# Kernel tuning notes

Measured on AMD Instinct MI355X. Metric: run time of the kernel, lower is better.

## Reference

```python
import jax, jax.numpy as jnp
import numpy as np

B, C, ROWS, COLS = 16, 1, 128, 128
E, H, L, VOCAB = 64, 32, 3, 258


def setup_inputs() -> dict:
    key = jax.random.key(0)
    ks = jax.random.split(key, 18)
    s = 0.05
    d = {
        "x": jax.random.randint(ks[0], (B, C, ROWS, COLS), 0, VOCAB, dtype=jnp.int32),
        "embed_table": jax.random.normal(ks[1], (VOCAB, E), jnp.float32) * s,
    }
    in_sizes = [E + 1, H, H]
    k = 2
    for l in range(L):
        d[f"w_ih_l{l}"] = jax.random.normal(ks[k], (3 * H, in_sizes[l]), jnp.float32) * s; k += 1
        d[f"w_hh_l{l}"] = jax.random.normal(ks[k], (3 * H, H), jnp.float32) * s; k += 1
        d[f"b_ih_l{l}"] = jax.random.normal(ks[k], (3 * H,), jnp.float32) * s; k += 1
        d[f"b_hh_l{l}"] = jax.random.normal(ks[k], (3 * H,), jnp.float32) * s; k += 1
    d["w_h2e"] = jax.random.normal(ks[14], (E + 1, H), jnp.float32) * s
    d["b_h2e"] = jax.random.normal(ks[15], (E + 1,), jnp.float32) * s
    d["w_out"] = jax.random.normal(ks[16], (VOCAB, H), jnp.float32) * s
    d["b_out"] = jax.random.normal(ks[17], (VOCAB,), jnp.float32) * s
    return d


def _forward(x, embed_table, wih, whh, bih, bhh, w_h2e, b_h2e, w_out, b_out):
    b, c, rows, cols = x.shape
    T = cols * c  # GRU sequence length per row
    Hh = whh[0].shape[1]
    nL = len(wih)

    xf = x.reshape(b, rows, T)
    emb = embed_table[xf]  # [B, rows, T, E]
    # normalized row coordinate in [-1, 1), appended as extra feature
    row_pos = jnp.arange(rows, dtype=emb.dtype) / rows * 2.0 - 1.0
    row_feat = jnp.broadcast_to(row_pos[None, :, None, None], (b, rows, T, 1))
    xin = jnp.concatenate([emb, row_feat], axis=-1)  # [B, rows, T, E+1]

    def gru_step(h, x_t):
        # h: [L, B, H]; x_t: [B, E+1]. torch GRU gate order: r, z, n.
        inp = x_t
        hs = []
        for l in range(nL):
            gi = inp @ wih[l].T + bih[l]
            gh = h[l] @ whh[l].T + bhh[l]
            ir, iz, inn = jnp.split(gi, 3, axis=-1)
            hr, hz, hn = jnp.split(gh, 3, axis=-1)
            r = jax.nn.sigmoid(ir + hr)
            z = jax.nn.sigmoid(iz + hz)
            n = jnp.tanh(inn + r * hn)
            hl = (1.0 - z) * n + z * h[l]
            hs.append(hl)
            inp = hl
        return jnp.stack(hs), inp  # emit top-layer output

    def row_step(prev_out, x_row):
        # prev_out: [B, T, H] top-layer GRU output of previous row
        comb = x_row + prev_out @ w_h2e.T + b_h2e  # [B, T, E+1]
        h0 = jnp.zeros((nL, b, Hh), comb.dtype)  # fresh h0 per row, as in torch
        _, out = jax.lax.scan(gru_step, h0, jnp.swapaxes(comb, 0, 1))  # [T, B, H]
        out = jnp.swapaxes(out, 0, 1)  # [B, T, H]
        return out, out

    prev0 = jnp.zeros((b, T, Hh), xin.dtype)
    _, outs = jax.lax.scan(row_step, prev0, jnp.swapaxes(xin, 0, 1))  # [rows, B, T, H]
    outs = jnp.swapaxes(outs, 0, 1)  # [B, rows, T, H]
    pred = outs @ w_out.T + b_out  # [B, rows, T, 258]
    return pred.reshape(b, c, rows, cols, VOCAB)


def reference(x, embed_table, w_ih_l0, w_hh_l0, b_ih_l0, b_hh_l0,
              w_ih_l1, w_hh_l1, b_ih_l1, b_hh_l1,
              w_ih_l2, w_hh_l2, b_ih_l2, b_hh_l2,
              w_h2e, b_h2e, w_out, b_out):
    return _forward(x, embed_table,
                    (w_ih_l0, w_ih_l1, w_ih_l2),
                    (w_hh_l0, w_hh_l1, w_hh_l2),
                    (b_ih_l0, b_ih_l1, b_ih_l2),
                    (b_hh_l0, b_hh_l1, b_hh_l2),
                    w_h2e, b_h2e, w_out, b_out)
```

## Files before the change

### kernel.cpp

```cpp
#include <hip/hip_runtime.h>
#include <math.h>

#define BATCH 16
#define RWS   128
#define TT    128
#define HH    32
#define GG    96
#define RPB   8
#define NRG   (RWS/RPB)
#define WSTR  34
#define FSTR  16

#define H2_BYTES   (BATCH*RWS*TT*HH*4)
#define FLAG_OFF   H2_BYTES
#define FLAG_BYTES (NRG*BATCH*FSTR*4)
#define PTAB_OFF   (FLAG_OFF + FLAG_BYTES)
#define WF_OFF     (PTAB_OFF + 258*GG*4)

__device__ __forceinline__ float sigm(float x) { return 1.0f / (1.0f + __expf(-x)); }
__device__ __forceinline__ float tanhfast(float x) {
  x = fminf(fmaxf(x, -15.0f), 15.0f);
  float e = __expf(2.0f * x);
  return (e - 1.0f) / (e + 1.0f);
}

__device__ __forceinline__ float dot32(const float* __restrict__ w, const float* __restrict__ v) {
  float a0 = 0.f, a1 = 0.f;
#pragma unroll
  for (int k = 0; k < HH; k += 4) {
    float2 w0 = *(const float2*)(w + k);
    float2 w1 = *(const float2*)(w + k + 2);
    float2 v0 = *(const float2*)(v + k);
    float2 v1 = *(const float2*)(v + k + 2);
    a0 = fmaf(w0.x, v0.x, fmaf(w0.y, v0.y, a0));
    a1 = fmaf(w1.x, v1.x, fmaf(w1.y, v1.y, a1));
  }
  return a0 + a1;
}

__global__ __launch_bounds__(128)
void prep_kernel(const float* __restrict__ emb, const float* __restrict__ wih0,
                 const float* __restrict__ bih0, const float* __restrict__ wh2e,
                 const float* __restrict__ bh2e, float* __restrict__ Ptab,
                 float* __restrict__ Wfo) {
  const int blk = blockIdx.x, tid = threadIdx.x;
  if (blk < 258) {
    if (tid < GG) {
      const float* wr = wih0 + tid * 65;
      const float* e  = emb + blk * 64;
      float acc = bih0[tid];
      for (int k = 0; k < 64; ++k) acc = fmaf(wr[k], e[k], acc);
      for (int k = 0; k < 65; ++k) acc = fmaf(wr[k], bh2e[k], acc);
      Ptab[blk * GG + tid] = acc;
    }
  } else {
    const int g = blk - 258;
    if (tid < HH) {
      const float* wr = wih0 + g * 65;
      float acc = 0.f;
      for (int k = 0; k < 65; ++k) acc = fmaf(wr[k], wh2e[k * HH + tid], acc);
      Wfo[g * HH + tid] = acc;
    }
  }
}

__device__ __forceinline__ void loadmat(const float* __restrict__ src, float* __restrict__ dst, int tid) {
  for (int i = tid; i < GG * HH; i += 256) dst[(i >> 5) * WSTR + (i & 31)] = src[i];
}

__global__ __launch_bounds__(256)
void rnn_kernel(const int* __restrict__ xg, const float* __restrict__ wih0,
                const float* __restrict__ whh0g, const float* __restrict__ bhh0g,
                const float* __restrict__ wih1g, const float* __restrict__ whh1g,
                const float* __restrict__ bih1g, const float* __restrict__ bhh1g,
                const float* __restrict__ wih2g, const float* __restrict__ whh2g,
                const float* __restrict__ bih2g, const float* __restrict__ bhh2g,
                const float* __restrict__ Ptab, const float* __restrict__ Wfg,
                float* __restrict__ h2buf, int* __restrict__ flags) {
  extern __shared__ float lds[];
  float* Wf    = lds;
  float* Whh0  = Wf   + GG * WSTR;
  float* Wih1  = Whh0 + GG * WSTR;
  float* Whh1  = Wih1 + GG * WSTR;
  float* Wih2  = Whh1 + GG * WSTR;
  float* Whh2  = Wih2 + GG * WSTR;
  float* bias  = Whh2 + GG * WSTR;
  float* prevs = bias + 5 * GG;
  float* h0s   = prevs + HH;
  float* h1s   = h0s + RPB * HH;
  float* h2a   = h1s + RPB * HH;
  float* h2b   = h2a + RPB * HH;

  const int tid = threadIdx.x;
  const int j   = tid & 31;
  const int s   = tid >> 5;
  const int g   = blockIdx.x >> 4;
  const int bat = blockIdx.x & 15;
  const int row = g * RPB + s;

  loadmat(Wfg,   Wf,   tid);
  loadmat(whh0g, Whh0, tid);
  loadmat(wih1g, Wih1, tid);
  loadmat(whh1g, Whh1, tid);
  loadmat(wih2g, Wih2, tid);
  loadmat(whh2g, Whh2, tid);
  for (int i = tid; i < GG; i += 256) {
    bias[i]          = bhh0g[i];
    bias[GG + i]     = bih1g[i];
    bias[2 * GG + i] = bhh1g[i];
    bias[3 * GG + i] = bih2g[i];
    bias[4 * GG + i] = bhh2g[i];
  }
  h0s[tid] = 0.f; h1s[tid] = 0.f; h2a[tid] = 0.f; h2b[tid] = 0.f;
  if (tid < HH) prevs[tid] = 0.f;

  const float rowpos = (float)row * (2.0f / 128.0f) - 1.0f;
  const float rpr = wih0[j * 65 + 64] * rowpos;
  const float rpz = wih0[(32 + j) * 65 + 64] * rowpos;
  const float rpn = wih0[(64 + j) * 65 + 64] * rowpos;
  __syncthreads();

  float h0r = 0.f, h1r = 0.f, h2r = 0.f;
  const size_t xbase = (size_t)(bat * RWS + row) * TT;
  const size_t obase = (size_t)(bat * RWS + row) * TT * HH + j;
  const size_t pbase = (row > 0) ? ((size_t)(bat * RWS + (row - 1)) * TT * HH + j) : 0;
  int* myflag = flags + (g * BATCH + bat) * FSTR;
  const int* pflag = flags + ((g > 0 ? g - 1 : 0) * BATCH + bat) * FSTR;
  const float* hb0 = h0s + s * HH;
  const float* hb1 = h1s + s * HH;

  int vcur = xg[xbase];

  for (int i = 0; i < TT + RPB - 1; ++i) {
    const int t = i - s;
    const bool act = (t >= 0) && (t < TT);
    const float* h2rd = (i & 1) ? h2a : h2b;
    float*       h2w  = (i & 1) ? h2b : h2a;

    const int tn = t + 1;
    const int vnext = (tn >= 0 && tn < TT) ? xg[xbase + tn] : 0;
    const float Pr = Ptab[vcur * GG + j];
    const float Pz = Ptab[vcur * GG + 32 + j];
    const float Pn = Ptab[vcur * GG + 64 + j];

    if (g > 0 && i < TT) {
      if (tid == 0) {
        const int want = i + 1;
        while (__hip_atomic_load(pflag, __ATOMIC_RELAXED, __HIP_MEMORY_SCOPE_AGENT) < want)
          __builtin_amdgcn_s_sleep(1);
      }
    }
    __syncthreads();

    if (s == 0 && g > 0 && act) {
      prevs[j] = __hip_atomic_load(h2buf + pbase + (size_t)t * HH,
                                   __ATOMIC_RELAXED, __HIP_MEMORY_SCOPE_AGENT);
    }

    if (act) {
      const float* hb2 = h2rd + s * HH;
      float ghr0 = bias[j]          + dot32(Whh0 + j * WSTR, hb0);
      float ghz0 = bias[32 + j]     + dot32(Whh0 + (32 + j) * WSTR, hb0);
      float ghn0 = bias[64 + j]     + dot32(Whh0 + (64 + j) * WSTR, hb0);
      float ghr1 = bias[2*GG + j]      + dot32(Whh1 + j * WSTR, hb1);
      float ghz1 = bias[2*GG + 32 + j] + dot32(Whh1 + (32 + j) * WSTR, hb1);
      float ghn1 = bias[2*GG + 64 + j] + dot32(Whh1 + (64 + j) * WSTR, hb1);
      float ghr2 = bias[4*GG + j]      + dot32(Whh2 + j * WSTR, hb2);
      float ghz2 = bias[4*GG + 32 + j] + dot32(Whh2 + (32 + j) * WSTR, hb2);
      float ghn2 = bias[4*GG + 64 + j] + dot32(Whh2 + (64 + j) * WSTR, hb2);

      const float* pb = (s == 0) ? prevs : (h2rd + (s - 1) * HH);
      {
        float gir = Pr + rpr + dot32(Wf + j * WSTR, pb);
        float giz = Pz + rpz + dot32(Wf + (32 + j) * WSTR, pb);
        float gin = Pn + rpn + dot32(Wf + (64 + j) * WSTR, pb);
        float rg = sigm(gir + ghr0);
        float zg = sigm(giz + ghz0);
        float ng = tanhfast(gin + rg * ghn0);
        h0r = (1.f - zg) * ng + zg * h0r;
      }
      h0s[s * HH + j] = h0r;

      {
        float gir = bias[GG + j]        + dot32(Wih1 + j * WSTR, hb0);
        float giz = bias[GG + 32 + j]   + dot32(Wih1 + (32 + j) * WSTR, hb0);
        float gin = bias[GG + 64 + j]   + dot32(Wih1 + (64 + j) * WSTR, hb0);
        float rg = sigm(gir + ghr1);
        float zg = sigm(giz + ghz1);
        float ng = tanhfast(gin + rg * ghn1);
        h1r = (1.f - zg) * ng + zg * h1r;
      }
      h1s[s * HH + j] = h1r;

      {
        float gir = bias[3*GG + j]        + dot32(Wih2 + j * WSTR, hb1);
        float giz = bias[3*GG + 32 + j]   + dot32(Wih2 + (32 + j) * WSTR, hb1);
        float gin = bias[3*GG + 64 + j]   + dot32(Wih2 + (64 + j) * WSTR, hb1);
        float rg = sigm(gir + ghr2);
        float zg = sigm(giz + ghz2);
        float ng = tanhfast(gin + rg * ghn2);
        h2r = (1.f - zg) * ng + zg * h2r;
      }
      h2w[s * HH + j] = h2r;

      if (s == RPB - 1) {
        __hip_atomic_store(h2buf + obase + (size_t)t * HH, h2r,
                           __ATOMIC_RELAXED, __HIP_MEMORY_SCOPE_AGENT);
      } else {
        h2buf[obase + (size_t)t * HH] = h2r;
      }
    }

    if (tid == 224 && i >= RPB - 1) {
      asm volatile("s_waitcnt vmcnt(0)" ::: "memory");
      __hip_atomic_store(myflag, i - (RPB - 2), __ATOMIC_RELAXED, __HIP_MEMORY_SCOPE_AGENT);
    }

    vcur = vnext;
  }
}

__global__ __launch_bounds__(256)
void proj_kernel(const float* __restrict__ h2buf, const float* __restrict__ wout,
                 const float* __restrict__ bout, float* __restrict__ out) {
  __shared__ float stage[32 * 258];
  const int tid = threadIdx.x;
  const int p = tid & 31, vq = tid >> 5;
  const size_t pos = (size_t)blockIdx.x * 32 + p;
  const float* hrow = h2buf + pos * HH;
  float h[HH];
#pragma unroll
  for (int k = 0; k < HH; k += 4) {
    float4 f = *(const float4*)(hrow + k);
    h[k] = f.x; h[k + 1] = f.y; h[k + 2] = f.z; h[k + 3] = f.w;
  }
#pragma unroll 1
  for (int vi = 0; vi <= 32; ++vi) {
    int v = vq + vi * 8;
    if (v < 258) {
      const float* wrow = wout + v * HH;
      float a0 = bout[v], a1 = 0.f;
#pragma unroll
      for (int k = 0; k < HH; k += 4) {
        float4 w = *(const float4*)(wrow + k);
        a0 = fmaf(w.x, h[k],     fmaf(w.y, h[k + 1], a0));
        a1 = fmaf(w.z, h[k + 2], fmaf(w.w, h[k + 3], a1));
      }
      stage[p * 258 + v] = a0 + a1;
    }
  }
  __syncthreads();
  float* o = out + (size_t)blockIdx.x * 32 * 258;
#pragma unroll 1
  for (int i = tid; i < 32 * 258; i += 256) o[i] = stage[i];
}

extern "C" void kernel_launch(void* const* d_in, const int* in_sizes, int n_in,
                              void* d_out, int out_size, void* d_ws, size_t ws_size,
                              hipStream_t stream) {
  const int*   x    = (const int*)d_in[0];
  const float* emb  = (const float*)d_in[1];
  const float* wih0 = (const float*)d_in[2];
  const float* whh0 = (const float*)d_in[3];
  const float* bih0 = (const float*)d_in[4];
  const float* bhh0 = (const float*)d_in[5];
  const float* wih1 = (const float*)d_in[6];
  const float* whh1 = (const float*)d_in[7];
  const float* bih1 = (const float*)d_in[8];
  const float* bhh1 = (const float*)d_in[9];
  const float* wih2 = (const float*)d_in[10];
  const float* whh2 = (const float*)d_in[11];
  const float* bih2 = (const float*)d_in[12];
  const float* bhh2 = (const float*)d_in[13];
  const float* wh2e = (const float*)d_in[14];
  const float* bh2e = (const float*)d_in[15];
  const float* wout = (const float*)d_in[16];
  const float* bout = (const float*)d_in[17];
  float* out = (float*)d_out;

  char*  ws    = (char*)d_ws;
  float* h2buf = (float*)ws;
  int*   flags = (int*)(ws + FLAG_OFF);
  float* Ptab  = (float*)(ws + PTAB_OFF);
  float* Wf    = (float*)(ws + WF_OFF);

  hipMemsetAsync(flags, 0, FLAG_BYTES, stream);
  prep_kernel<<<354, 128, 0, stream>>>(emb, wih0, bih0, wh2e, bh2e, Ptab, Wf);

  const int rnn_lds_bytes = (6 * GG * WSTR + 5 * GG + HH + 4 * RPB * HH) * 4;
  hipFuncSetAttribute((const void*)rnn_kernel,
                      hipFuncAttributeMaxDynamicSharedMemorySize, rnn_lds_bytes);
  rnn_kernel<<<NRG * BATCH, 256, rnn_lds_bytes, stream>>>(
      x, wih0, whh0, bhh0, wih1, whh1, bih1, bhh1, wih2, whh2, bih2, bhh2,
      Ptab, Wf, h2buf, flags);

  proj_kernel<<<8192, 256, 0, stream>>>(h2buf, wout, bout, out);
}
```

Baseline: 1.830 ms.

## Pack GRU weights per unit, hoist hidden vectors to registers, prefetch cross-block inputs

Repacks each weight matrix so the three gate rows of a unit sit contiguously with a 100-float stride and can be read as float4. The hidden-state vectors are pulled into registers once per step and reused across all gate dot products, and biases are kept in registers. The previous row-group's output is prefetched one step ahead, the flag is published at the top of the loop, and a lighter barrier skips polling when the flag is already far enough ahead. The aim is fewer LDS reads per step and less synchronisation latency on the serial recurrence, at the cost of higher register pressure and more delicate flag ordering.

New measurement: 1.678 ms. 1.09x faster.

```diff
diff --git a/kernel.cpp b/kernel.cpp
--- a/kernel.cpp
+++ b/kernel.cpp
@@ -8,7 +8,7 @@
 #define GG    96
 #define RPB   8
 #define NRG   (RWS/RPB)
-#define WSTR  34
+#define WP    100
 #define FSTR  16
 
 #define H2_BYTES   (BATCH*RWS*TT*HH*4)
@@ -24,18 +24,30 @@
   return (e - 1.0f) / (e + 1.0f);
 }
 
-__device__ __forceinline__ float dot32(const float* __restrict__ w, const float* __restrict__ v) {
-  float a0 = 0.f, a1 = 0.f;
-#pragma unroll
-  for (int k = 0; k < HH; k += 4) {
-    float2 w0 = *(const float2*)(w + k);
-    float2 w1 = *(const float2*)(w + k + 2);
-    float2 v0 = *(const float2*)(v + k);
-    float2 v1 = *(const float2*)(v + k + 2);
-    a0 = fmaf(w0.x, v0.x, fmaf(w0.y, v0.y, a0));
-    a1 = fmaf(w1.x, v1.x, fmaf(w1.y, v1.y, a1));
-  }
-  return a0 + a1;
+__device__ __forceinline__ void barrier_lgkm() {
+  __builtin_amdgcn_sched_barrier(0);
+  asm volatile("s_waitcnt lgkmcnt(0)" ::: "memory");
+  __builtin_amdgcn_s_barrier();
+  __builtin_amdgcn_sched_barrier(0);
+}
+
+__device__ __forceinline__ float dot32p(const float4* __restrict__ w, const float4 v[8]) {
+  float a0 = 0.f, a1 = 0.f, a2 = 0.f, a3 = 0.f;
+#pragma unroll
+  for (int c = 0; c < 8; ++c) {
+    float4 W = w[c];
+    a0 = fmaf(W.x, v[c].x, a0);
+    a1 = fmaf(W.y, v[c].y, a1);
+    a2 = fmaf(W.z, v[c].z, a2);
+    a3 = fmaf(W.w, v[c].w, a3);
+  }
+  return (a0 + a1) + (a2 + a3);
+}
+
+__device__ __forceinline__ void hoist8(float4 dst[8], const float* __restrict__ src) {
+  const float4* p = (const float4*)src;
+#pragma unroll
+  for (int c = 0; c < 8; ++c) dst[c] = p[c];
 }
 
 __global__ __launch_bounds__(128)
@@ -64,11 +76,16 @@
   }
 }
 
-__device__ __forceinline__ void loadmat(const float* __restrict__ src, float* __restrict__ dst, int tid) {
-  for (int i = tid; i < GG * HH; i += 256) dst[(i >> 5) * WSTR + (i & 31)] = src[i];
-}
-
-__global__ __launch_bounds__(256)
+__device__ __forceinline__ void loadmat_packed(const float* __restrict__ src,
+                                               float* __restrict__ dst, int tid) {
+  for (int i = tid; i < GG * HH; i += 256) {
+    const int g = i >> 5, k = i & 31;
+    const int gate = g >> 5, j = g & 31;
+    dst[j * WP + gate * 32 + k] = src[g * 32 + k];
+  }
+}
+
+__global__ __launch_bounds__(256, 1)
 void rnn_kernel(const int* __restrict__ xg, const float* __restrict__ wih0,
                 const float* __restrict__ whh0g, const float* __restrict__ bhh0g,
                 const float* __restrict__ wih1g, const float* __restrict__ whh1g,
@@ -77,15 +94,14 @@
                 const float* __restrict__ bih2g, const float* __restrict__ bhh2g,
                 const float* __restrict__ Ptab, const float* __restrict__ Wfg,
                 float* __restrict__ h2buf, int* __restrict__ flags) {
-  extern __shared__ float lds[];
+  extern __shared__ __align__(16) float lds[];
   float* Wf    = lds;
-  float* Whh0  = Wf   + GG * WSTR;
-  float* Wih1  = Whh0 + GG * WSTR;
-  float* Whh1  = Wih1 + GG * WSTR;
-  float* Wih2  = Whh1 + GG * WSTR;
-  float* Whh2  = Wih2 + GG * WSTR;
-  float* bias  = Whh2 + GG * WSTR;
-  float* prevs = bias + 5 * GG;
+  float* Whh0  = Wf   + HH * WP;
+  float* Wih1  = Whh0 + HH * WP;
+  float* Whh1  = Wih1 + HH * WP;
+  float* Wih2  = Whh1 + HH * WP;
+  float* Whh2  = Wih2 + HH * WP;
+  float* prevs = Whh2 + HH * WP;
   float* h0s   = prevs + HH;
   float* h1s   = h0s + RPB * HH;
   float* h2a   = h1s + RPB * HH;
@@ -98,22 +114,20 @@
   const int bat = blockIdx.x & 15;
   const int row = g * RPB + s;
 
-  loadmat(Wfg,   Wf,   tid);
-  loadmat(whh0g, Whh0, tid);
-  loadmat(wih1g, Wih1, tid);
-  loadmat(whh1g, Whh1, tid);
-  loadmat(wih2g, Wih2, tid);
-  loadmat(whh2g, Whh2, tid);
-  for (int i = tid; i < GG; i += 256) {
-    bias[i]          = bhh0g[i];
-    bias[GG + i]     = bih1g[i];
-    bias[2 * GG + i] = bhh1g[i];
-    bias[3 * GG + i] = bih2g[i];
-    bias[4 * GG + i] = bhh2g[i];
-  }
+  loadmat_packed(Wfg,   Wf,   tid);
+  loadmat_packed(whh0g, Whh0, tid);
+  loadmat_packed(wih1g, Wih1, tid);
+  loadmat_packed(whh1g, Whh1, tid);
+  loadmat_packed(wih2g, Wih2, tid);
+  loadmat_packed(whh2g, Whh2, tid);
   h0s[tid] = 0.f; h1s[tid] = 0.f; h2a[tid] = 0.f; h2b[tid] = 0.f;
   if (tid < HH) prevs[tid] = 0.f;
 
+  const float bh0r = bhh0g[j], bh0z = bhh0g[32 + j], bh0n = bhh0g[64 + j];
+  const float bi1r = bih1g[j], bi1z = bih1g[32 + j], bi1n = bih1g[64 + j];
+  const float bh1r = bhh1g[j], bh1z = bhh1g[32 + j], bh1n = bhh1g[64 + j];
+  const float bi2r = bih2g[j], bi2z = bih2g[32 + j], bi2n = bih2g[64 + j];
+  const float bh2r_ = bhh2g[j], bh2z_ = bhh2g[32 + j], bh2n_ = bhh2g[64 + j];
   const float rowpos = (float)row * (2.0f / 128.0f) - 1.0f;
   const float rpr = wih0[j * 65 + 64] * rowpos;
   const float rpz = wih0[(32 + j) * 65 + 64] * rowpos;
@@ -121,15 +135,35 @@
   __syncthreads();
 
   float h0r = 0.f, h1r = 0.f, h2r = 0.f;
+  float4 Vh0[8], Vh1[8], Vh2[8], Vp[8];
+#pragma unroll
+  for (int c = 0; c < 8; ++c) {
+    Vh0[c] = make_float4(0.f, 0.f, 0.f, 0.f);
+    Vh1[c] = make_float4(0.f, 0.f, 0.f, 0.f);
+    Vh2[c] = make_float4(0.f, 0.f, 0.f, 0.f);
+  }
+
   const size_t xbase = (size_t)(bat * RWS + row) * TT;
   const size_t obase = (size_t)(bat * RWS + row) * TT * HH + j;
   const size_t pbase = (row > 0) ? ((size_t)(bat * RWS + (row - 1)) * TT * HH + j) : 0;
   int* myflag = flags + (g * BATCH + bat) * FSTR;
   const int* pflag = flags + ((g > 0 ? g - 1 : 0) * BATCH + bat) * FSTR;
-  const float* hb0 = h0s + s * HH;
-  const float* hb1 = h1s + s * HH;
 
   int vcur = xg[xbase];
+  float pvq = 0.f;
+  int lastF = 0;
+
+  if (g > 0) {
+    if (tid == 0) {
+      int f;
+      do { f = __hip_atomic_load(pflag, __ATOMIC_RELAXED, __HIP_MEMORY_SCOPE_AGENT); }
+      while (f < 1);
+      lastF = f;
+    }
+    __syncthreads();
+    if (s == 0)
+      pvq = __hip_atomic_load(h2buf + pbase, __ATOMIC_RELAXED, __HIP_MEMORY_SCOPE_AGENT);
+  }
 
   for (int i = 0; i < TT + RPB - 1; ++i) {
     const int t = i - s;
@@ -137,71 +171,81 @@
     const float* h2rd = (i & 1) ? h2a : h2b;
     float*       h2w  = (i & 1) ? h2b : h2a;
 
+    if (tid == 224 && i >= RPB) {
+      asm volatile("s_waitcnt vmcnt(0)" ::: "memory");
+      __hip_atomic_store(myflag, i - (RPB - 1), __ATOMIC_RELAXED, __HIP_MEMORY_SCOPE_AGENT);
+    }
+
     const int tn = t + 1;
     const int vnext = (tn >= 0 && tn < TT) ? xg[xbase + tn] : 0;
     const float Pr = Ptab[vcur * GG + j];
     const float Pz = Ptab[vcur * GG + 32 + j];
     const float Pn = Ptab[vcur * GG + 64 + j];
 
-    if (g > 0 && i < TT) {
-      if (tid == 0) {
-        const int want = i + 1;
-        while (__hip_atomic_load(pflag, __ATOMIC_RELAXED, __HIP_MEMORY_SCOPE_AGENT) < want)
-          __builtin_amdgcn_s_sleep(1);
-      }
-    }
-    __syncthreads();
-
-    if (s == 0 && g > 0 && act) {
-      prevs[j] = __hip_atomic_load(h2buf + pbase + (size_t)t * HH,
-                                   __ATOMIC_RELAXED, __HIP_MEMORY_SCOPE_AGENT);
+    if (g > 0 && i < TT - 1) {
+      if (tid == 0 && lastF < i + 2) {
+        int f;
+        do { f = __hip_atomic_load(pflag, __ATOMIC_RELAXED, __HIP_MEMORY_SCOPE_AGENT); }
+        while (f < i + 2);
+        lastF = f;
+      }
+    }
+    barrier_lgkm();
+
+    if (s == 0 && g > 0) {
+      if (act) prevs[j] = pvq;
+      if (i + 1 < TT)
+        pvq = __hip_atomic_load(h2buf + pbase + (size_t)(i + 1) * HH,
+                                __ATOMIC_RELAXED, __HIP_MEMORY_SCOPE_AGENT);
     }
 
     if (act) {
-      const float* hb2 = h2rd + s * HH;
-      float ghr0 = bias[j]          + dot32(Whh0 + j * WSTR, hb0);
-      float ghz0 = bias[32 + j]     + dot32(Whh0 + (32 + j) * WSTR, hb0);
-      float ghn0 = bias[64 + j]     + dot32(Whh0 + (64 + j) * WSTR, hb0);
-      float ghr1 = bias[2*GG + j]      + dot32(Whh1 + j * WSTR, hb1);
-      float ghz1 = bias[2*GG + 32 + j] + dot32(Whh1 + (32 + j) * WSTR, hb1);
-      float ghn1 = bias[2*GG + 64 + j] + dot32(Whh1 + (64 + j) * WSTR, hb1);
-      float ghr2 = bias[4*GG + j]      + dot32(Whh2 + j * WSTR, hb2);
-      float ghz2 = bias[4*GG + 32 + j] + dot32(Whh2 + (32 + j) * WSTR, hb2);
-      float ghn2 = bias[4*GG + 64 + j] + dot32(Whh2 + (64 + j) * WSTR, hb2);
-
-      const float* pb = (s == 0) ? prevs : (h2rd + (s - 1) * HH);
+      const float ghr0 = bh0r + dot32p((const float4*)(Whh0 + j * WP),      Vh0);
+      const float ghz0 = bh0z + dot32p((const float4*)(Whh0 + j * WP + 32), Vh0);
+      const float ghn0 = bh0n + dot32p((const float4*)(Whh0 + j * WP + 64), Vh0);
+      const float ghr1 = bh1r + dot32p((const float4*)(Whh1 + j * WP),      Vh1);
+      const float ghz1 = bh1z + dot32p((const float4*)(Whh1 + j * WP + 32), Vh1);
+      const float ghn1 = bh1n + dot32p((const float4*)(Whh1 + j * WP + 64), Vh1);
+      const float ghr2 = bh2r_ + dot32p((const float4*)(Whh2 + j * WP),      Vh2);
+      const float ghz2 = bh2z_ + dot32p((const float4*)(Whh2 + j * WP + 32), Vh2);
+      const float ghn2 = bh2n_ + dot32p((const float4*)(Whh2 + j * WP + 64), Vh2);
+
+      hoist8(Vp, (s == 0) ? prevs : (h2rd + (s - 1) * HH));
       {
-        float gir = Pr + rpr + dot32(Wf + j * WSTR, pb);
-        float giz = Pz + rpz + dot32(Wf + (32 + j) * WSTR, pb);
-        float gin = Pn + rpn + dot32(Wf + (64 + j) * WSTR, pb);
-        float rg = sigm(gir + ghr0);
-        float zg = sigm(giz + ghz0);
-        float ng = tanhfast(gin + rg * ghn0);
+        const float gir = Pr + rpr + dot32p((const float4*)(Wf + j * WP),      Vp);
+        const float giz = Pz + rpz + dot32p((const float4*)(Wf + j * WP + 32), Vp);
+        const float gin = Pn + rpn + dot32p((const float4*)(Wf + j * WP + 64), Vp);
+        const float rg = sigm(gir + ghr0);
+        const float zg = sigm(giz + ghz0);
+        const float ng = tanhfast(gin + rg * ghn0);
         h0r = (1.f - zg) * ng + zg * h0r;
       }
       h0s[s * HH + j] = h0r;
+      hoist8(Vh0, h0s + s * HH);
 
       {
-        float gir = bias[GG + j]        + dot32(Wih1 + j * WSTR, hb0);
-        float giz = bias[GG + 32 + j]   + dot32(Wih1 + (32 + j) * WSTR, hb0);
-        float gin = bias[GG + 64 + j]   + dot32(Wih1 + (64 + j) * WSTR, hb0);
-        float rg = sigm(gir + ghr1);
-        float zg = sigm(giz + ghz1);
-        float ng = tanhfast(gin + rg * ghn1);
+        const float gir = bi1r + dot32p((const float4*)(Wih1 + j * WP),      Vh0);
+        const float giz = bi1z + dot32p((const float4*)(Wih1 + j * WP + 32), Vh0);
+        const float gin = bi1n + dot32p((const float4*)(Wih1 + j * WP + 64), Vh0);
+        const float rg = sigm(gir + ghr1);
+        const float zg = sigm(giz + ghz1);
+        const float ng = tanhfast(gin + rg * ghn1);
         h1r = (1.f - zg) * ng + zg * h1r;
       }
       h1s[s * HH + j] = h1r;
+      hoist8(Vh1, h1s + s * HH);
 
       {
-        float gir = bias[3*GG + j]        + dot32(Wih2 + j * WSTR, hb1);
-        float giz = bias[3*GG + 32 + j]   + dot32(Wih2 + (32 + j) * WSTR, hb1);
-        float gin = bias[3*GG + 64 + j]   + dot32(Wih2 + (64 + j) * WSTR, hb1);
-        float rg = sigm(gir + ghr2);
-        float zg = sigm(giz + ghz2);
-        float ng = tanhfast(gin + rg * ghn2);
+        const float gir = bi2r + dot32p((const float4*)(Wih2 + j * WP),      Vh1);
+        const float giz = bi2z + dot32p((const float4*)(Wih2 + j * WP + 32), Vh1);
+        const float gin = bi2n + dot32p((const float4*)(Wih2 + j * WP + 64), Vh1);
+        const float rg = sigm(gir + ghr2);
+        const float zg = sigm(giz + ghz2);
+        const float ng = tanhfast(gin + rg * ghn2);
         h2r = (1.f - zg) * ng + zg * h2r;
       }
       h2w[s * HH + j] = h2r;
+      hoist8(Vh2, h2w + s * HH);
 
       if (s == RPB - 1) {
         __hip_atomic_store(h2buf + obase + (size_t)t * HH, h2r,
@@ -211,12 +255,12 @@
       }
     }
 
-    if (tid == 224 && i >= RPB - 1) {
-      asm volatile("s_waitcnt vmcnt(0)" ::: "memory");
-      __hip_atomic_store(myflag, i - (RPB - 2), __ATOMIC_RELAXED, __HIP_MEMORY_SCOPE_AGENT);
-    }
-
     vcur = vnext;
+  }
+
+  if (tid == 224) {
+    asm volatile("s_waitcnt vmcnt(0)" ::: "memory");
+    __hip_atomic_store(myflag, TT, __ATOMIC_RELAXED, __HIP_MEMORY_SCOPE_AGENT);
   }
 }
 
@@ -287,7 +331,7 @@
   hipMemsetAsync(flags, 0, FLAG_BYTES, stream);
   prep_kernel<<<354, 128, 0, stream>>>(emb, wih0, bih0, wh2e, bh2e, Ptab, Wf);
 
-  const int rnn_lds_bytes = (6 * GG * WSTR + 5 * GG + HH + 4 * RPB * HH) * 4;
+  const int rnn_lds_bytes = (6 * HH * WP + HH + 4 * RPB * HH) * 4;
   hipFuncSetAttribute((const void*)rnn_kernel,
                       hipFuncAttributeMaxDynamicSharedMemorySize, rnn_lds_bytes);
   rnn_kernel<<<NRG * BATCH, 256, rnn_lds_bytes, stream>>>(
```
